# Kernel tuning notes

Measured on AMD Instinct MI355X. Metric: run time of the kernel, lower is better.

Reference implementation:

```python
import jax, jax.numpy as jnp
import numpy as np

N, D, B, K, DOUT = 100000, 128, 500000, 3, 128


def setup_inputs() -> dict:
    key = jax.random.key(0)
    k1, k2, k3 = jax.random.split(key, 3)
    x = jax.random.normal(k1, (N, D), dtype=jnp.float32)
    indices = jax.random.randint(k2, (B, K), 0, N, dtype=jnp.int64)
    # xavier_normal_ for weight [D*(K+1), DOUT]
    fan_in, fan_out = D * (K + 1), DOUT
    std = float(np.sqrt(2.0 / (fan_in + fan_out)))
    weight = jax.random.normal(k3, (fan_in, fan_out), dtype=jnp.float32) * std
    return {"x": x, "indices": indices, "weight": weight}


def reference(x, indices, weight):
    # _1_to_k, cfg='default', normalize=False
    # gather K node rows per hyperedge and concat: [B, K*D]
    x_nonpool = x[indices].reshape(indices.shape[0], -1)
    w_nonpool = weight[:-D]          # [K*D, DOUT]
    w_pool = weight[-D:]             # [D, DOUT]
    x_pool = jnp.sum(x, axis=0, keepdims=True)  # [1, D] (sum since normalize=False)
    return x_nonpool @ w_nonpool + x_pool @ w_pool  # [B, DOUT]
```

## Files before the change

kernel.cpp:

```cpp
#include <hip/hip_runtime.h>
#include <stdint.h>

#define NROWS 100000
#define DIMD  128
#define KKIDX 3
#define NDOUT 128
#define KDIM  384
#define NBAT  500000

typedef float  f4v  __attribute__((ext_vector_type(4)));
typedef short  s8v  __attribute__((ext_vector_type(8)));

__device__ __forceinline__ short f2bf(float f) {
    union { float f; uint32_t u; } c; c.f = f;
    uint32_t u = c.u;
    uint32_t r = (u + 0x7FFFu + ((u >> 16) & 1u)) >> 16;
    return (short)r;
}

__global__ void k_wt(const float* __restrict__ w, unsigned short* __restrict__ wT) {
    int g = blockIdx.x * 256 + threadIdx.x;
    if (g >= KDIM * NDOUT) return;
    int k = g >> 7;
    int n = g & 127;
    wT[n * KDIM + k] = (unsigned short)f2bf(w[g]);
}

template<bool WRITE_BF>
__global__ void k_colsum(const float* __restrict__ x, float* __restrict__ xpool,
                         unsigned short* __restrict__ xbf) {
    __shared__ float red[256];
    int col  = threadIdx.x & 127;
    int half = threadIdx.x >> 7;
    float acc = 0.f;
    int r0 = blockIdx.x * 250;
    for (int r = r0 + half; r < r0 + 250; r += 2) {
        float v = x[r * DIMD + col];
        acc += v;
        if (WRITE_BF) xbf[r * DIMD + col] = (unsigned short)f2bf(v);
    }
    red[threadIdx.x] = acc;
    __syncthreads();
    if (threadIdx.x < 128)
        atomicAdd(&xpool[col], red[threadIdx.x] + red[threadIdx.x + 128]);
}

__global__ void k_pool(const float* __restrict__ xpool, const float* __restrict__ w,
                       float* __restrict__ pool_out) {
    int j = threadIdx.x;
    float acc = 0.f;
    for (int d = 0; d < DIMD; ++d)
        acc += xpool[d] * w[(KDIM + d) * NDOUT + j];
    pool_out[j] = acc;
}

#define LSTR 200

template<bool XBF>
__global__ __launch_bounds__(512, 2)
void k_main(const float* __restrict__ x, const unsigned short* __restrict__ xbf,
            const int* __restrict__ idx, const unsigned short* __restrict__ wT,
            const float* __restrict__ pool, float* __restrict__ out) {
    __shared__ short wlds[128 * LSTR];
    const int tid  = threadIdx.x;
    const int wave = tid >> 6;
    const int lane = tid & 63;
    const int quad = lane >> 4;
    const int l16  = lane & 15;

    const int rowb = blockIdx.x * 512 + wave * 64;

    int goff[4][3];
    #pragma unroll
    for (int mt = 0; mt < 4; ++mt) {
        int r = rowb + mt * 16 + l16;
        if (r >= NBAT) r = NBAT - 1;
        #pragma unroll
        for (int s = 0; s < KKIDX; ++s)
            goff[mt][s] = idx[r * 3 + s] * DIMD;
    }

    f4v acc[4][8];
    #pragma unroll
    for (int mt = 0; mt < 4; ++mt)
        #pragma unroll
        for (int nt = 0; nt < 8; ++nt) {
            f4v z = {0.f, 0.f, 0.f, 0.f};
            acc[mt][nt] = z;
        }

    const int sn   = tid >> 2;
    const int sseg = tid & 3;

    for (int p = 0; p < 2; ++p) {
        __syncthreads();
        #pragma unroll
        for (int j = 0; j < 12; ++j) {
            int k = sseg * 48 + j * 4;
            const unsigned short* src = wT + sn * KDIM + p * 192 + k;
            *(uint2*)(&wlds[sn * LSTR + k]) = *(const uint2*)src;
        }
        __syncthreads();

        #pragma unroll
        for (int ks = 0; ks < 6; ++ks) {
            const int kstep = p * 6 + ks;
            const int srci  = kstep >> 2;
            const int colb  = (kstep & 3) * 32 + quad * 8;

            s8v aF[4];
            #pragma unroll
            for (int mt = 0; mt < 4; ++mt) {
                if (XBF) {
                    aF[mt] = *(const s8v*)(xbf + goff[mt][srci] + colb);
                } else {
                    const float* ap = x + goff[mt][srci] + colb;
                    f4v v0 = *(const f4v*)ap;
                    f4v v1 = *(const f4v*)(ap + 4);
                    s8v a;
                    a[0] = f2bf(v0[0]); a[1] = f2bf(v0[1]);
                    a[2] = f2bf(v0[2]); a[3] = f2bf(v0[3]);
                    a[4] = f2bf(v1[0]); a[5] = f2bf(v1[1]);
                    a[6] = f2bf(v1[2]); a[7] = f2bf(v1[3]);
                    aF[mt] = a;
                }
            }

            const int krow = ks * 32 + quad * 8;
            s8v bF[8];
            #pragma unroll
            for (int nt = 0; nt < 8; ++nt)
                bF[nt] = *(const s8v*)(&wlds[(nt * 16 + l16) * LSTR + krow]);

            #pragma unroll
            for (int mt = 0; mt < 4; ++mt)
                #pragma unroll
                for (int nt = 0; nt < 8; ++nt)
                    acc[mt][nt] = __builtin_amdgcn_mfma_f32_16x16x32_bf16(
                        aF[mt], bF[nt], acc[mt][nt], 0, 0, 0);
        }
    }

    #pragma unroll
    for (int nt = 0; nt < 8; ++nt) {
        float pv = pool[nt * 16 + l16];
        #pragma unroll
        for (int mt = 0; mt < 4; ++mt) {
            int r0 = rowb + mt * 16 + quad * 4;
            #pragma unroll
            for (int i = 0; i < 4; ++i) {
                int r = r0 + i;
                if (r < NBAT)
                    out[r * NDOUT + nt * 16 + l16] = acc[mt][nt][i] + pv;
            }
        }
    }
}

extern "C" void kernel_launch(void* const* d_in, const int* in_sizes, int n_in,
                              void* d_out, int out_size, void* d_ws, size_t ws_size,
                              hipStream_t stream) {
    const float* x   = (const float*)d_in[0];
    const int*   idx = (const int*)d_in[1];
    const float* w   = (const float*)d_in[2];
    float*       out = (float*)d_out;

    char* ws = (char*)d_ws;
    float* xpool           = (float*)ws;
    float* pool_out        = (float*)(ws + 512);
    unsigned short* wT     = (unsigned short*)(ws + 1024);
    unsigned short* xbf    = (unsigned short*)(ws + 99328);
    const size_t NEED_BIG  = 99328 + (size_t)NROWS * DIMD * 2;
    const bool big = ws_size >= NEED_BIG;

    hipMemsetAsync(xpool, 0, 512, stream);
    if (big) k_colsum<true ><<<400, 256, 0, stream>>>(x, xpool, xbf);
    else     k_colsum<false><<<400, 256, 0, stream>>>(x, xpool, xbf);
    k_wt  <<<192, 256, 0, stream>>>(w, wT);
    k_pool<<<1, 128, 0, stream>>>(xpool, w, pool_out);

    const int grid = (NBAT + 511) / 512;
    if (big) k_main<true ><<<grid, 512, 0, stream>>>(x, xbf, idx, wT, pool_out, out);
    else     k_main<false><<<grid, 512, 0, stream>>>(x, xbf, idx, wT, pool_out, out);
}
```

Measured before the change: 466.8 us.

## Halve rows per wave, prefetch gathered A fragments, swap MFMA operands for vector stores

Each block now covers 256 rows (32 per wave) rather than 512, and launch bounds rise to 4 blocks per CU, which cuts accumulator registers and is meant to raise occupancy for hiding gather latency. The gathered A fragments for the next k-step are loaded one step ahead (register double-buffering). MFMA operands are swapped so each lane holds four consecutive output columns, allowing 16-byte nontemporal output stores. Weight staging into LDS now uses 16-byte loads. The trade-off is that the weight tile is loaded into LDS twice as often per row, and the B fragments are reused across fewer rows.

Result: faster. 442.7 us (-5.2%).

```diff
diff --git a/kernel.cpp b/kernel.cpp
--- a/kernel.cpp
+++ b/kernel.cpp
@@ -10,6 +10,7 @@
 
 typedef float  f4v  __attribute__((ext_vector_type(4)));
 typedef short  s8v  __attribute__((ext_vector_type(8)));
+typedef unsigned int u4v __attribute__((ext_vector_type(4)));
 
 __device__ __forceinline__ short f2bf(float f) {
     union { float f; uint32_t u; } c; c.f = f;
@@ -57,7 +58,7 @@
 #define LSTR 200
 
 template<bool XBF>
-__global__ __launch_bounds__(512, 2)
+__global__ __launch_bounds__(512, 4)
 void k_main(const float* __restrict__ x, const unsigned short* __restrict__ xbf,
             const int* __restrict__ idx, const unsigned short* __restrict__ wT,
             const float* __restrict__ pool, float* __restrict__ out) {
@@ -68,11 +69,11 @@
     const int quad = lane >> 4;
     const int l16  = lane & 15;
 
-    const int rowb = blockIdx.x * 512 + wave * 64;
-
-    int goff[4][3];
-    #pragma unroll
-    for (int mt = 0; mt < 4; ++mt) {
+    const int rowb = blockIdx.x * 256 + wave * 32;
+
+    int goff[2][KKIDX];
+    #pragma unroll
+    for (int mt = 0; mt < 2; ++mt) {
         int r = rowb + mt * 16 + l16;
         if (r >= NBAT) r = NBAT - 1;
         #pragma unroll
@@ -80,9 +81,9 @@
             goff[mt][s] = idx[r * 3 + s] * DIMD;
     }
 
-    f4v acc[4][8];
-    #pragma unroll
-    for (int mt = 0; mt < 4; ++mt)
+    f4v acc[2][8];
+    #pragma unroll
+    for (int mt = 0; mt < 2; ++mt)
         #pragma unroll
         for (int nt = 0; nt < 8; ++nt) {
             f4v z = {0.f, 0.f, 0.f, 0.f};
@@ -92,66 +93,90 @@
     const int sn   = tid >> 2;
     const int sseg = tid & 3;
 
+    s8v aC[2];
+    #pragma unroll
+    for (int mt = 0; mt < 2; ++mt) {
+        if (XBF) {
+            aC[mt] = *(const s8v*)(xbf + goff[mt][0] + quad * 8);
+        } else {
+            const float* ap = x + goff[mt][0] + quad * 8;
+            f4v v0 = *(const f4v*)ap;
+            f4v v1 = *(const f4v*)(ap + 4);
+            s8v a;
+            a[0] = f2bf(v0[0]); a[1] = f2bf(v0[1]);
+            a[2] = f2bf(v0[2]); a[3] = f2bf(v0[3]);
+            a[4] = f2bf(v1[0]); a[5] = f2bf(v1[1]);
+            a[6] = f2bf(v1[2]); a[7] = f2bf(v1[3]);
+            aC[mt] = a;
+        }
+    }
+
+    #pragma unroll
     for (int p = 0; p < 2; ++p) {
         __syncthreads();
         #pragma unroll
-        for (int j = 0; j < 12; ++j) {
-            int k = sseg * 48 + j * 4;
-            const unsigned short* src = wT + sn * KDIM + p * 192 + k;
-            *(uint2*)(&wlds[sn * LSTR + k]) = *(const uint2*)src;
+        for (int j = 0; j < 6; ++j) {
+            int k = sseg * 48 + j * 8;
+            *(u4v*)(&wlds[sn * LSTR + k]) = *(const u4v*)(wT + sn * KDIM + p * 192 + k);
         }
         __syncthreads();
 
         #pragma unroll
         for (int ks = 0; ks < 6; ++ks) {
             const int kstep = p * 6 + ks;
-            const int srci  = kstep >> 2;
-            const int colb  = (kstep & 3) * 32 + quad * 8;
-
-            s8v aF[4];
-            #pragma unroll
-            for (int mt = 0; mt < 4; ++mt) {
-                if (XBF) {
-                    aF[mt] = *(const s8v*)(xbf + goff[mt][srci] + colb);
-                } else {
-                    const float* ap = x + goff[mt][srci] + colb;
-                    f4v v0 = *(const f4v*)ap;
-                    f4v v1 = *(const f4v*)(ap + 4);
-                    s8v a;
-                    a[0] = f2bf(v0[0]); a[1] = f2bf(v0[1]);
-                    a[2] = f2bf(v0[2]); a[3] = f2bf(v0[3]);
-                    a[4] = f2bf(v1[0]); a[5] = f2bf(v1[1]);
-                    a[6] = f2bf(v1[2]); a[7] = f2bf(v1[3]);
-                    aF[mt] = a;
+
+            s8v aN[2];
+            if (kstep < 11) {
+                const int kn   = kstep + 1;
+                const int srci = kn >> 2;
+                const int colb = (kn & 3) * 32 + quad * 8;
+                #pragma unroll
+                for (int mt = 0; mt < 2; ++mt) {
+                    if (XBF) {
+                        aN[mt] = *(const s8v*)(xbf + goff[mt][srci] + colb);
+                    } else {
+                        const float* ap = x + goff[mt][srci] + colb;
+                        f4v v0 = *(const f4v*)ap;
+                        f4v v1 = *(const f4v*)(ap + 4);
+                        s8v a;
+                        a[0] = f2bf(v0[0]); a[1] = f2bf(v0[1]);
+                        a[2] = f2bf(v0[2]); a[3] = f2bf(v0[3]);
+                        a[4] = f2bf(v1[0]); a[5] = f2bf(v1[1]);
+                        a[6] = f2bf(v1[2]); a[7] = f2bf(v1[3]);
+                        aN[mt] = a;
+                    }
                 }
             }
 
             const int krow = ks * 32 + quad * 8;
-            s8v bF[8];
             #pragma unroll
-            for (int nt = 0; nt < 8; ++nt)
-                bF[nt] = *(const s8v*)(&wlds[(nt * 16 + l16) * LSTR + krow]);
-
-            #pragma unroll
-            for (int mt = 0; mt < 4; ++mt)
+            for (int h = 0; h < 2; ++h) {
+                s8v bF[4];
                 #pragma unroll
-                for (int nt = 0; nt < 8; ++nt)
-                    acc[mt][nt] = __builtin_amdgcn_mfma_f32_16x16x32_bf16(
-                        aF[mt], bF[nt], acc[mt][nt], 0, 0, 0);
+                for (int q = 0; q < 4; ++q)
+                    bF[q] = *(const s8v*)(&wlds[((h * 4 + q) * 16 + l16) * LSTR + krow]);
+                #pragma unroll
+                for (int mt = 0; mt < 2; ++mt)
+                    #pragma unroll
+                    for (int q = 0; q < 4; ++q)
+                        acc[mt][h * 4 + q] = __builtin_amdgcn_mfma_f32_16x16x32_bf16(
+                            bF[q], aC[mt], acc[mt][h * 4 + q], 0, 0, 0);
+            }
+
+            if (kstep < 11) { aC[0] = aN[0]; aC[1] = aN[1]; }
         }
     }
 
     #pragma unroll
     for (int nt = 0; nt < 8; ++nt) {
-        float pv = pool[nt * 16 + l16];
-        #pragma unroll
-        for (int mt = 0; mt < 4; ++mt) {
-            int r0 = rowb + mt * 16 + quad * 4;
-            #pragma unroll
-            for (int i = 0; i < 4; ++i) {
-                int r = r0 + i;
-                if (r < NBAT)
-                    out[r * NDOUT + nt * 16 + l16] = acc[mt][nt][i] + pv;
+        f4v pv = *(const f4v*)(pool + nt * 16 + quad * 4);
+        #pragma unroll
+        for (int mt = 0; mt < 2; ++mt) {
+            int r = rowb + mt * 16 + l16;
+            if (r < NBAT) {
+                f4v v = acc[mt][nt] + pv;
+                __builtin_nontemporal_store(v,
+                    (f4v*)(out + (size_t)r * NDOUT + nt * 16 + quad * 4));
             }
         }
     }
@@ -179,7 +204,7 @@
     k_wt  <<<192, 256, 0, stream>>>(w, wT);
     k_pool<<<1, 128, 0, stream>>>(xpool, w, pool_out);
 
-    const int grid = (NBAT + 511) / 512;
+    const int grid = (NBAT + 255) / 256;
     if (big) k_main<true ><<<grid, 512, 0, stream>>>(x, xbf, idx, wT, pool_out, out);
     else     k_main<false><<<grid, 512, 0, stream>>>(x, xbf, idx, wT, pool_out, out);
 }
```
